# Performance work log

Measured on AMD Instinct MI355X. Metric: run time of the kernel, lower is better.

The kernel has to match this reference:

```python
import jax, jax.numpy as jnp
import numpy as np

# Dimensions
B, D, C, E = 4096, 1024, 512, 16            # batch, embedding_dim, context_dim, n_experts
LIN, R, LOUT = 1024, 16, 1024               # lora_dim = (in, r, out)
H_GATE, H_EXP, Z = 2048, 2048, 512          # gating hidden, expert hidden, expert out


def setup_inputs() -> dict:
    key = jax.random.key(0)
    ks = jax.random.split(key, 12)
    sc = 0.02
    return {
        "s": jax.random.normal(ks[0], (B, D), jnp.float32),
        "c": jax.random.normal(ks[1], (B, C), jnp.float32),
        # gating_model: Linear(D,2048) -> ReLU -> Linear(2048,E) -> Softmax
        "Wg1": jax.random.normal(ks[2], (D, H_GATE), jnp.float32) * sc,
        "bg1": jnp.zeros((H_GATE,), jnp.float32),
        "Wg2": jax.random.normal(ks[3], (H_GATE, E), jnp.float32) * sc,
        "bg2": jnp.zeros((E,), jnp.float32),
        # experts (stacked): Linear(D+C,2048) -> ReLU -> Linear(2048,512)
        "We1": jax.random.normal(ks[4], (E, D + C, H_EXP), jnp.float32) * sc,
        "be1": jnp.zeros((E, H_EXP), jnp.float32),
        "We2": jax.random.normal(ks[5], (E, H_EXP, Z), jnp.float32) * sc,
        "be2": jnp.zeros((E, Z), jnp.float32),
        # LoRA decode heads
        "WA": jax.random.normal(ks[6], (Z, LIN * R), jnp.float32) * sc,
        "bA": jnp.zeros((LIN * R,), jnp.float32),
        "WB": jax.random.normal(ks[7], (Z, R * LOUT), jnp.float32) * sc,
        "bB": jnp.zeros((R * LOUT,), jnp.float32),
    }


def reference(s, c, Wg1, bg1, Wg2, bg2, We1, be1, We2, be2, WA, bA, WB, bB):
    x = jnp.concatenate([s, c], axis=-1)                         # (B, D+C)
    # gating: softmax over experts
    gates = jax.nn.softmax(jnp.maximum(s @ Wg1 + bg1, 0.0) @ Wg2 + bg2, axis=-1)  # (B, E)
    # all-expert dense 2-layer MLPs (soft MoE)
    h = jnp.maximum(jnp.einsum('bd,edh->ebh', x, We1) + be1[:, None, :], 0.0)     # (E, B, H_EXP)
    eo = jnp.einsum('ebh,ehz->ebz', h, We2) + be2[:, None, :]                     # (E, B, Z)
    # gating-weighted sum over experts
    z = jnp.einsum('be,ebz->bz', gates, eo)                      # (B, Z)
    # LoRA decode heads, reshaped per batch element
    A = (z @ WA + bA).reshape(B, LIN, R)
    Bm = (z @ WB + bB).reshape(B, R, LOUT)
    return (A, Bm)
```

## Files before the change

### kernel.cpp

```cpp
#include <hip/hip_runtime.h>
#include <stdint.h>

typedef __attribute__((ext_vector_type(4))) float f32x4;
typedef __attribute__((ext_vector_type(8))) __bf16 bf16x8;

__device__ __forceinline__ ushort f2bf(float f) {
  union { float f; uint32_t u; } v; v.f = f;
  uint32_t r = v.u + 0x7fffu + ((v.u >> 16) & 1u);
  return (ushort)(r >> 16);
}
__device__ __forceinline__ float bf2f(uint32_t h) {
  union { uint32_t u; float f; } v; v.u = h << 16;
  return v.f;
}

__device__ __forceinline__ void gload16(const void* g, const void* l) {
  __builtin_amdgcn_global_load_lds(
      (const __attribute__((address_space(1))) void*)(uintptr_t)g,
      (__attribute__((address_space(3))) void*)(uint32_t)(uintptr_t)l,
      16, 0, 0);
}

template<int EPI, int COL>
__global__ __launch_bounds__(512, 1)
void gemm256p(const ushort* __restrict__ A, const ushort* __restrict__ Bt,
              const float* __restrict__ bias, const float* __restrict__ bias2,
              void* __restrict__ outp,
              int K, int lda, int ldb, int ldo,
              size_t aStride, size_t bStride, int biasStride, size_t oStride,
              const float* __restrict__ gates)
{
  __shared__ __attribute__((aligned(16))) char smem[3 * 32768];

  const int bx = COL ? blockIdx.y : blockIdx.x;
  const int by = COL ? blockIdx.x : blockIdx.y;
  const int eb = blockIdx.z;

  const int t    = threadIdx.x;
  const int lane = t & 63;
  const int wid  = t >> 6;
  const int wr   = wid >> 2, wc = wid & 3;
  const int fr   = lane & 15, fq = lane >> 4;

  const int r  = t >> 2;
  const int jc = (t & 3) ^ ((t >> 3) & 3);
  const ushort* Ae = A  + aStride * eb;
  const ushort* Be = Bt + bStride * eb;
  const ushort* sA0 = Ae + (size_t)(by * 256 + (r >> 6) * 128 +   0 + (r & 63)) * lda + jc * 8;
  const ushort* sA1 = Ae + (size_t)(by * 256 + (r >> 6) * 128 +  64 + (r & 63)) * lda + jc * 8;
  const ushort* sB0 = Be + (size_t)(bx * 256 +   0 + r) * ldb + jc * 8;
  const ushort* sB1 = Be + (size_t)(bx * 256 + 128 + r) * ldb + jc * 8;
  const int dT = t * 16;

  const int swz  = (fq ^ ((fr >> 1) & 3)) * 16;
  const int aOff = (wr * 64 + fr) * 64 + swz;
  const int bOff = 16384 + (wc * 64 + fr) * 64 + swz;

  f32x4 acc[8][4];
#pragma unroll
  for (int m = 0; m < 8; ++m)
#pragma unroll
    for (int n = 0; n < 4; ++n) acc[m][n] = (f32x4){0.f, 0.f, 0.f, 0.f};

  const int NT = K >> 5;

#pragma unroll
  for (int kt = 0; kt < 2; ++kt) {
    char* d = smem + kt * 32768;
    gload16(sA0 + kt * 32, d + dT);
    gload16(sB0 + kt * 32, d + 16384 + dT);
    gload16(sB1 + kt * 32, d + 24576 + dT);
    gload16(sA1 + kt * 32, d + 8192 + dT);
  }
  asm volatile("s_waitcnt vmcnt(5)" ::: "memory");
  __builtin_amdgcn_s_barrier();

  int sc = 0;
  for (int T = 0; T < NT; ++T) {
    const char* base = smem + sc * 32768;
    const int ssi = (sc + 2 >= 3) ? sc - 1 : sc + 2;
    char* d = smem + ssi * 32768;
    const bool pf = (T + 2 < NT);
    const int ko = (T + 2) * 32;

    if (T < NT - 1) asm volatile("s_waitcnt vmcnt(4)" ::: "memory");
    else            asm volatile("s_waitcnt vmcnt(0)" ::: "memory");
    bf16x8 afA[4], bfv[4];
#pragma unroll
    for (int m = 0; m < 4; ++m) afA[m] = *(const bf16x8*)(base + aOff + m * 1024);
#pragma unroll
    for (int n = 0; n < 4; ++n) bfv[n] = *(const bf16x8*)(base + bOff + n * 1024);
    if (pf) { gload16(sA0 + ko, d + dT); gload16(sB0 + ko, d + 16384 + dT); }
    __builtin_amdgcn_sched_barrier(0);
    __builtin_amdgcn_s_barrier();
    __builtin_amdgcn_s_setprio(1);
#pragma unroll
    for (int m = 0; m < 4; ++m)
#pragma unroll
      for (int n = 0; n < 4; ++n)
        acc[m][n] = __builtin_amdgcn_mfma_f32_16x16x32_bf16(afA[m], bfv[n], acc[m][n], 0, 0, 0);
    __builtin_amdgcn_s_setprio(0);

    if (T < NT - 2)       asm volatile("s_waitcnt vmcnt(3)" ::: "memory");
    else if (T == NT - 2) asm volatile("s_waitcnt vmcnt(1)" ::: "memory");
    else                  asm volatile("s_waitcnt vmcnt(0)" ::: "memory");
    bf16x8 afB[4];
#pragma unroll
    for (int m = 0; m < 4; ++m) afB[m] = *(const bf16x8*)(base + 8192 + aOff + m * 1024);
    if (pf) { gload16(sB1 + ko, d + 24576 + dT); gload16(sA1 + ko, d + 8192 + dT); }
    __builtin_amdgcn_sched_barrier(0);
    __builtin_amdgcn_s_barrier();
    __builtin_amdgcn_s_setprio(1);
#pragma unroll
    for (int m = 0; m < 4; ++m)
#pragma unroll
      for (int n = 0; n < 4; ++n)
        acc[4 + m][n] = __builtin_amdgcn_mfma_f32_16x16x32_bf16(afB[m], bfv[n], acc[4 + m][n], 0, 0, 0);
    __builtin_amdgcn_s_setprio(0);

    sc = (sc + 1 == 3) ? 0 : sc + 1;
  }

  const int grow0 = by * 256 + wr * 128 + fq * 4;
  const int gcol0 = bx * 256 + wc * 64 + fr;

  if (EPI == 0) {
    ushort* oo = (ushort*)outp + oStride * eb;
    const float* bb = bias + (size_t)biasStride * eb;
#pragma unroll
    for (int n = 0; n < 4; ++n) {
      const int cc = gcol0 + n * 16;
      const float bv = bb[cc];
#pragma unroll
      for (int m = 0; m < 8; ++m) {
        const int rb = grow0 + (m >> 2) * 64 + (m & 3) * 16;
#pragma unroll
        for (int j = 0; j < 4; ++j) {
          const float v = acc[m][n][j] + bv;
          oo[(size_t)(rb + j) * ldo + cc] = f2bf(v > 0.f ? v : 0.f);
        }
      }
    }
  } else if (EPI == 2) {
    ushort* oo = (ushort*)outp + oStride * eb;
    const float* bb = bias + (size_t)biasStride * eb;
    float gv[8][4];
#pragma unroll
    for (int m = 0; m < 8; ++m) {
      const int rb = grow0 + (m >> 2) * 64 + (m & 3) * 16;
#pragma unroll
      for (int j = 0; j < 4; ++j) gv[m][j] = gates[(size_t)(rb + j) * 16 + eb];
    }
#pragma unroll
    for (int n = 0; n < 4; ++n) {
      const int cc = gcol0 + n * 16;
      const float bv = bb[cc];
#pragma unroll
      for (int m = 0; m < 8; ++m) {
        const int rb = grow0 + (m >> 2) * 64 + (m & 3) * 16;
#pragma unroll
        for (int j = 0; j < 4; ++j) {
          const float v = acc[m][n][j] + bv;
          oo[(size_t)(rb + j) * ldo + cc] = f2bf(v > 0.f ? gv[m][j] * v : 0.f);
        }
      }
    }
  } else if (EPI == 4) {
    float* oo = (float*)outp + oStride * eb;
#pragma unroll
    for (int n = 0; n < 4; ++n) {
      const int cc = gcol0 + n * 16;
#pragma unroll
      for (int m = 0; m < 8; ++m) {
        const int rb = grow0 + (m >> 2) * 64 + (m & 3) * 16;
#pragma unroll
        for (int j = 0; j < 4; ++j)
          oo[(size_t)(rb + j) * ldo + cc] = acc[m][n][j];
      }
    }
  } else {
    const bool second = (gcol0 >= ldo);
    const float* bp = second ? bias2 : bias;
    float* oo = (float*)outp + (second ? oStride : 0);
#pragma unroll
    for (int n = 0; n < 4; ++n) {
      const int cc = gcol0 + n * 16 - (second ? ldo : 0);
      const float bv = bp[cc];
#pragma unroll
      for (int m = 0; m < 8; ++m) {
        const int rb = grow0 + (m >> 2) * 64 + (m & 3) * 16;
#pragma unroll
        for (int j = 0; j < 4; ++j)
          oo[(size_t)(rb + j) * ldo + cc] = acc[m][n][j] + bv;
      }
    }
  }
}

__global__ __launch_bounds__(256)
void transpose_cvt(const float* __restrict__ in, ushort* __restrict__ out,
                   int K, int N, size_t inStride, size_t outStride)
{
  __shared__ float tile[64][65];
  const float* I = in + inStride * blockIdx.z;
  ushort* O = out + outStride * blockIdx.z;
  const int n0 = blockIdx.x * 64, k0 = blockIdx.y * 64;
  const int t = threadIdx.x;
  const int r = t >> 4, cv = (t & 15) * 4;
#pragma unroll
  for (int pp = 0; pp < 4; ++pp) {
    const int kr = r + pp * 16;
    const float4 v = *(const float4*)&I[(size_t)(k0 + kr) * N + (n0 + cv)];
    tile[kr][cv] = v.x; tile[kr][cv + 1] = v.y; tile[kr][cv + 2] = v.z; tile[kr][cv + 3] = v.w;
  }
  __syncthreads();
#pragma unroll
  for (int pp = 0; pp < 4; ++pp) {
    const int nr = r + pp * 16;
    ushort4 o4;
    o4.x = f2bf(tile[cv + 0][nr]); o4.y = f2bf(tile[cv + 1][nr]);
    o4.z = f2bf(tile[cv + 2][nr]); o4.w = f2bf(tile[cv + 3][nr]);
    *(ushort4*)&O[(size_t)(n0 + nr) * K + (k0 + cv)] = o4;
  }
}

__global__ __launch_bounds__(256)
void build_x(const float* __restrict__ s, const float* __restrict__ c, ushort* __restrict__ x)
{
  const size_t i = (size_t)blockIdx.x * 256 + threadIdx.x;
  const size_t b = i / 192;
  const int col  = (int)(i % 192) * 8;
  const float* src = (col < 1024) ? (s + b * 1024 + col) : (c + b * 512 + (col - 1024));
  const float4 v0 = ((const float4*)src)[0];
  const float4 v1 = ((const float4*)src)[1];
  uint4 o;
  o.x = f2bf(v0.x) | ((uint32_t)f2bf(v0.y) << 16);
  o.y = f2bf(v0.z) | ((uint32_t)f2bf(v0.w) << 16);
  o.z = f2bf(v1.x) | ((uint32_t)f2bf(v1.y) << 16);
  o.w = f2bf(v1.z) | ((uint32_t)f2bf(v1.w) << 16);
  *(uint4*)(x + i * 8) = o;
}

__global__ __launch_bounds__(256)
void reduce_z8(const float* __restrict__ zs, const float* __restrict__ gates,
               const float* __restrict__ be2, ushort* __restrict__ zb)
{
  const size_t i = ((size_t)blockIdx.x * 256 + threadIdx.x) * 4;
  const size_t S = (size_t)4096 * 512;
  const int rrow = (int)(i >> 9);
  const int ccol = (int)(i & 511);
  float4 sv = {0.f, 0.f, 0.f, 0.f};
#pragma unroll
  for (int p = 0; p < 8; ++p) {
    const float4 v = *(const float4*)(zs + (size_t)p * S + i);
    sv.x += v.x; sv.y += v.y; sv.z += v.z; sv.w += v.w;
  }
#pragma unroll
  for (int e = 0; e < 16; ++e) {
    const float ge = gates[(size_t)rrow * 16 + e];
    const float4 bv = *(const float4*)(be2 + (size_t)e * 512 + ccol);
    sv.x += ge * bv.x; sv.y += ge * bv.y; sv.z += ge * bv.z; sv.w += ge * bv.w;
  }
  ushort4 o4;
  o4.x = f2bf(sv.x); o4.y = f2bf(sv.y); o4.z = f2bf(sv.z); o4.w = f2bf(sv.w);
  *(ushort4*)(zb + i) = o4;
}

__global__ __launch_bounds__(256)
void gating2_softmax(const ushort* __restrict__ hg, const float* __restrict__ Wg2,
                     const float* __restrict__ bg2, float* __restrict__ gates)
{
  const int row  = (int)((blockIdx.x * 256 + threadIdx.x) >> 6);
  const int lane = threadIdx.x & 63;
  float acc[16];
#pragma unroll
  for (int e = 0; e < 16; ++e) acc[e] = 0.f;
  const ushort* hrow = hg + (size_t)row * 2048;
#pragma unroll
  for (int it = 0; it < 4; ++it) {
    const int kb = it * 512 + lane * 8;
    const uint4 pk = *(const uint4*)(hrow + kb);
    float hv[8] = { bf2f(pk.x & 0xffffu), bf2f(pk.x >> 16),
                    bf2f(pk.y & 0xffffu), bf2f(pk.y >> 16),
                    bf2f(pk.z & 0xffffu), bf2f(pk.z >> 16),
                    bf2f(pk.w & 0xffffu), bf2f(pk.w >> 16) };
#pragma unroll
    for (int j = 0; j < 8; ++j) {
      const float* wrow = Wg2 + (size_t)(kb + j) * 16;
#pragma unroll
      for (int e = 0; e < 16; ++e) acc[e] += hv[j] * wrow[e];
    }
  }
#pragma unroll
  for (int e = 0; e < 16; ++e) {
#pragma unroll
    for (int off = 32; off > 0; off >>= 1) acc[e] += __shfl_xor(acc[e], off);
    acc[e] += bg2[e];
  }
  float mx = acc[0];
#pragma unroll
  for (int e = 1; e < 16; ++e) mx = fmaxf(mx, acc[e]);
  float sum = 0.f;
#pragma unroll
  for (int e = 0; e < 16; ++e) { acc[e] = __expf(acc[e] - mx); sum += acc[e]; }
  const float inv = 1.f / sum;
  if (lane == 0) {
#pragma unroll
    for (int e = 0; e < 16; ++e) gates[(size_t)row * 16 + e] = acc[e] * inv;
  }
}

extern "C" void kernel_launch(void* const* d_in, const int* in_sizes, int n_in,
                              void* d_out, int out_size, void* d_ws, size_t ws_size,
                              hipStream_t stream)
{
  (void)in_sizes; (void)n_in; (void)out_size; (void)ws_size;
  const float* s   = (const float*)d_in[0];
  const float* c   = (const float*)d_in[1];
  const float* Wg1 = (const float*)d_in[2];
  const float* bg1 = (const float*)d_in[3];
  const float* Wg2 = (const float*)d_in[4];
  const float* bg2 = (const float*)d_in[5];
  const float* We1 = (const float*)d_in[6];
  const float* be1 = (const float*)d_in[7];
  const float* We2 = (const float*)d_in[8];
  const float* be2 = (const float*)d_in[9];
  const float* WA  = (const float*)d_in[10];
  const float* bA  = (const float*)d_in[11];
  const float* WB  = (const float*)d_in[12];
  const float* bB  = (const float*)d_in[13];
  float* out = (float*)d_out;

  char* ws = (char*)d_ws;
  size_t off = 0;
  auto alloc = [&](size_t bytes) {
    void* p = ws + off; off += (bytes + 255) & ~(size_t)255; return p;
  };
  ushort* x      = (ushort*)alloc((size_t)4096 * 1536 * 2);
  ushort* We1T   = (ushort*)alloc((size_t)16 * 2048 * 1536 * 2);
  ushort* We2cat = (ushort*)alloc((size_t)512 * 32768 * 2);
  ushort* WABT   = (ushort*)alloc((size_t)32768 * 512 * 2);
  float*  gates  = (float*)alloc((size_t)4096 * 16 * 4);
  float*  zsplit = (float*)alloc((size_t)8 * 4096 * 512 * 4);
  ushort* zb     = (ushort*)alloc((size_t)4096 * 512 * 2);
  ushort* h      = (ushort*)alloc((size_t)4096 * 32768 * 2);
  ushort* Wg1T = h;
  ushort* hg   = (ushort*)((char*)h + (size_t)2048 * 1024 * 2);

  const size_t S_We1 = (size_t)2048 * 1536;
  const size_t S_We2 = (size_t)512 * 2048;
  const size_t S_z   = (size_t)4096 * 512;

  build_x<<<3072, 256, 0, stream>>>(s, c, x);
  transpose_cvt<<<dim3(32, 16, 1),  256, 0, stream>>>(Wg1, Wg1T, 1024, 2048, 0, 0);
  transpose_cvt<<<dim3(32, 24, 16), 256, 0, stream>>>(We1, We1T, 1536, 2048, S_We1, S_We1);
  transpose_cvt<<<dim3(8, 32, 16),  256, 0, stream>>>(We2, We2cat, 32768, 512, S_We2, 2048);
  transpose_cvt<<<dim3(256, 8, 1),  256, 0, stream>>>(WA, WABT, 512, 16384, 0, 0);
  transpose_cvt<<<dim3(256, 8, 1),  256, 0, stream>>>(WB, WABT + (size_t)16384 * 512, 512, 16384, 0, 0);

  gemm256p<0, 1><<<dim3(16, 8, 1), 512, 0, stream>>>(x, Wg1T, bg1, nullptr, hg,
      1024, 1536, 1024, 2048, 0, 0, 0, 0, nullptr);
  gating2_softmax<<<1024, 256, 0, stream>>>(hg, Wg2, bg2, gates);

  gemm256p<2, 1><<<dim3(16, 8, 16), 512, 0, stream>>>(x, We1T, be1, nullptr, h,
      1536, 1536, 1536, 32768, 0, S_We1, 2048, 2048, gates);

  gemm256p<4, 0><<<dim3(2, 16, 8), 512, 0, stream>>>(h, We2cat, be2, nullptr, zsplit,
      4096, 32768, 32768, 512, 4096, 4096, 0, S_z, nullptr);

  reduce_z8<<<2048, 256, 0, stream>>>(zsplit, gates, be2, zb);

  gemm256p<3, 1><<<dim3(16, 128, 1), 512, 0, stream>>>(zb, WABT, bA, bB, out,
      512, 512, 512, 16384, 0, 0, 0, (size_t)4096 * 16384, nullptr);
}
```

Before: 1.181 ms.

## Restructure GEMM main loop barriers, vectorize epilogue stores, double split-K

The GEMM main loop moves each barrier ahead of its LDS fragment reads and prefetch issue, and the waitcnt thresholds are reworked to match. The MFMA operands are swapped so each lane holds four consecutive output columns, which lets the epilogues emit 4-wide vector stores and bias loads instead of scalar ones. The expert-down GEMM's split-K factor goes from 8 to 16 to give more blocks, at the cost of a larger fp32 partial buffer and more reads in the reduction kernel. These changes touch synchronization, output layout and work partitioning together.

```diff
diff --git a/kernel.cpp b/kernel.cpp
--- a/kernel.cpp
+++ b/kernel.cpp
@@ -72,8 +72,6 @@
     gload16(sB1 + kt * 32, d + 24576 + dT);
     gload16(sA1 + kt * 32, d + 8192 + dT);
   }
-  asm volatile("s_waitcnt vmcnt(5)" ::: "memory");
-  __builtin_amdgcn_s_barrier();
 
   int sc = 0;
   for (int T = 0; T < NT; ++T) {
@@ -83,115 +81,106 @@
     const bool pf = (T + 2 < NT);
     const int ko = (T + 2) * 32;
 
-    if (T < NT - 1) asm volatile("s_waitcnt vmcnt(4)" ::: "memory");
-    else            asm volatile("s_waitcnt vmcnt(0)" ::: "memory");
-    bf16x8 afA[4], bfv[4];
-#pragma unroll
-    for (int m = 0; m < 4; ++m) afA[m] = *(const bf16x8*)(base + aOff + m * 1024);
-#pragma unroll
-    for (int n = 0; n < 4; ++n) bfv[n] = *(const bf16x8*)(base + bOff + n * 1024);
+    if (T < NT - 1) asm volatile("s_waitcnt vmcnt(5)" ::: "memory");
+    else            asm volatile("s_waitcnt vmcnt(1)" ::: "memory");
+    __builtin_amdgcn_s_barrier();
     if (pf) { gload16(sA0 + ko, d + dT); gload16(sB0 + ko, d + 16384 + dT); }
-    __builtin_amdgcn_sched_barrier(0);
+
+    bf16x8 af[4], bf[4];
+#pragma unroll
+    for (int m = 0; m < 4; ++m) af[m] = *(const bf16x8*)(base + aOff + m * 1024);
+#pragma unroll
+    for (int n = 0; n < 4; ++n) bf[n] = *(const bf16x8*)(base + bOff + n * 1024);
+
+    __builtin_amdgcn_s_setprio(1);
+#pragma unroll
+    for (int m = 0; m < 4; ++m)
+#pragma unroll
+      for (int n = 0; n < 4; ++n)
+        acc[m][n] = __builtin_amdgcn_mfma_f32_16x16x32_bf16(bf[n], af[m], acc[m][n], 0, 0, 0);
+    __builtin_amdgcn_s_setprio(0);
+
+    if (T < NT - 2)       asm volatile("s_waitcnt vmcnt(6)" ::: "memory");
+    else if (T == NT - 2) asm volatile("s_waitcnt vmcnt(4)" ::: "memory");
+    else                  asm volatile("s_waitcnt vmcnt(0)" ::: "memory");
     __builtin_amdgcn_s_barrier();
+    if (pf) { gload16(sB1 + ko, d + 24576 + dT); gload16(sA1 + ko, d + 8192 + dT); }
+
+#pragma unroll
+    for (int m = 0; m < 4; ++m) af[m] = *(const bf16x8*)(base + 8192 + aOff + m * 1024);
     __builtin_amdgcn_s_setprio(1);
 #pragma unroll
     for (int m = 0; m < 4; ++m)
 #pragma unroll
       for (int n = 0; n < 4; ++n)
-        acc[m][n] = __builtin_amdgcn_mfma_f32_16x16x32_bf16(afA[m], bfv[n], acc[m][n], 0, 0, 0);
+        acc[4 + m][n] = __builtin_amdgcn_mfma_f32_16x16x32_bf16(bf[n], af[m], acc[4 + m][n], 0, 0, 0);
     __builtin_amdgcn_s_setprio(0);
 
-    if (T < NT - 2)       asm volatile("s_waitcnt vmcnt(3)" ::: "memory");
-    else if (T == NT - 2) asm volatile("s_waitcnt vmcnt(1)" ::: "memory");
-    else                  asm volatile("s_waitcnt vmcnt(0)" ::: "memory");
-    bf16x8 afB[4];
-#pragma unroll
-    for (int m = 0; m < 4; ++m) afB[m] = *(const bf16x8*)(base + 8192 + aOff + m * 1024);
-    if (pf) { gload16(sB1 + ko, d + 24576 + dT); gload16(sA1 + ko, d + 8192 + dT); }
-    __builtin_amdgcn_sched_barrier(0);
-    __builtin_amdgcn_s_barrier();
-    __builtin_amdgcn_s_setprio(1);
-#pragma unroll
-    for (int m = 0; m < 4; ++m)
-#pragma unroll
-      for (int n = 0; n < 4; ++n)
-        acc[4 + m][n] = __builtin_amdgcn_mfma_f32_16x16x32_bf16(afB[m], bfv[n], acc[4 + m][n], 0, 0, 0);
-    __builtin_amdgcn_s_setprio(0);
-
     sc = (sc + 1 == 3) ? 0 : sc + 1;
   }
 
-  const int grow0 = by * 256 + wr * 128 + fq * 4;
-  const int gcol0 = bx * 256 + wc * 64 + fr;
+  const int grow0 = by * 256 + wr * 128 + fr;
+  const int gcol0 = bx * 256 + wc * 64 + fq * 4;
 
   if (EPI == 0) {
     ushort* oo = (ushort*)outp + oStride * eb;
     const float* bb = bias + (size_t)biasStride * eb;
 #pragma unroll
-    for (int n = 0; n < 4; ++n) {
-      const int cc = gcol0 + n * 16;
-      const float bv = bb[cc];
-#pragma unroll
-      for (int m = 0; m < 8; ++m) {
-        const int rb = grow0 + (m >> 2) * 64 + (m & 3) * 16;
-#pragma unroll
-        for (int j = 0; j < 4; ++j) {
-          const float v = acc[m][n][j] + bv;
-          oo[(size_t)(rb + j) * ldo + cc] = f2bf(v > 0.f ? v : 0.f);
-        }
+    for (int m = 0; m < 8; ++m) {
+      const int Mr = grow0 + (m >> 2) * 64 + (m & 3) * 16;
+#pragma unroll
+      for (int n = 0; n < 4; ++n) {
+        const int Nc = gcol0 + n * 16;
+        const f32x4 bv = *(const f32x4*)&bb[Nc];
+        ushort4 o4;
+        float v0 = acc[m][n][0] + bv[0]; float v1 = acc[m][n][1] + bv[1];
+        float v2 = acc[m][n][2] + bv[2]; float v3 = acc[m][n][3] + bv[3];
+        o4.x = f2bf(v0 > 0.f ? v0 : 0.f); o4.y = f2bf(v1 > 0.f ? v1 : 0.f);
+        o4.z = f2bf(v2 > 0.f ? v2 : 0.f); o4.w = f2bf(v3 > 0.f ? v3 : 0.f);
+        *(ushort4*)&oo[(size_t)Mr * ldo + Nc] = o4;
       }
     }
   } else if (EPI == 2) {
     ushort* oo = (ushort*)outp + oStride * eb;
     const float* bb = bias + (size_t)biasStride * eb;
-    float gv[8][4];
 #pragma unroll
     for (int m = 0; m < 8; ++m) {
-      const int rb = grow0 + (m >> 2) * 64 + (m & 3) * 16;
-#pragma unroll
-      for (int j = 0; j < 4; ++j) gv[m][j] = gates[(size_t)(rb + j) * 16 + eb];
-    }
-#pragma unroll
-    for (int n = 0; n < 4; ++n) {
-      const int cc = gcol0 + n * 16;
-      const float bv = bb[cc];
-#pragma unroll
-      for (int m = 0; m < 8; ++m) {
-        const int rb = grow0 + (m >> 2) * 64 + (m & 3) * 16;
-#pragma unroll
-        for (int j = 0; j < 4; ++j) {
-          const float v = acc[m][n][j] + bv;
-          oo[(size_t)(rb + j) * ldo + cc] = f2bf(v > 0.f ? gv[m][j] * v : 0.f);
-        }
+      const int Mr = grow0 + (m >> 2) * 64 + (m & 3) * 16;
+      const float g = gates[(size_t)Mr * 16 + eb];
+#pragma unroll
+      for (int n = 0; n < 4; ++n) {
+        const int Nc = gcol0 + n * 16;
+        const f32x4 bv = *(const f32x4*)&bb[Nc];
+        ushort4 o4;
+        float v0 = acc[m][n][0] + bv[0]; float v1 = acc[m][n][1] + bv[1];
+        float v2 = acc[m][n][2] + bv[2]; float v3 = acc[m][n][3] + bv[3];
+        o4.x = f2bf(v0 > 0.f ? g * v0 : 0.f); o4.y = f2bf(v1 > 0.f ? g * v1 : 0.f);
+        o4.z = f2bf(v2 > 0.f ? g * v2 : 0.f); o4.w = f2bf(v3 > 0.f ? g * v3 : 0.f);
+        *(ushort4*)&oo[(size_t)Mr * ldo + Nc] = o4;
       }
     }
   } else if (EPI == 4) {
     float* oo = (float*)outp + oStride * eb;
 #pragma unroll
-    for (int n = 0; n < 4; ++n) {
-      const int cc = gcol0 + n * 16;
-#pragma unroll
-      for (int m = 0; m < 8; ++m) {
-        const int rb = grow0 + (m >> 2) * 64 + (m & 3) * 16;
-#pragma unroll
-        for (int j = 0; j < 4; ++j)
-          oo[(size_t)(rb + j) * ldo + cc] = acc[m][n][j];
-      }
+    for (int m = 0; m < 8; ++m) {
+      const int Mr = grow0 + (m >> 2) * 64 + (m & 3) * 16;
+#pragma unroll
+      for (int n = 0; n < 4; ++n)
+        *(f32x4*)&oo[(size_t)Mr * ldo + gcol0 + n * 16] = acc[m][n];
     }
   } else {
     const bool second = (gcol0 >= ldo);
     const float* bp = second ? bias2 : bias;
     float* oo = (float*)outp + (second ? oStride : 0);
-#pragma unroll
-    for (int n = 0; n < 4; ++n) {
-      const int cc = gcol0 + n * 16 - (second ? ldo : 0);
-      const float bv = bp[cc];
-#pragma unroll
-      for (int m = 0; m < 8; ++m) {
-        const int rb = grow0 + (m >> 2) * 64 + (m & 3) * 16;
-#pragma unroll
-        for (int j = 0; j < 4; ++j)
-          oo[(size_t)(rb + j) * ldo + cc] = acc[m][n][j] + bv;
+    const int cb = second ? ldo : 0;
+#pragma unroll
+    for (int m = 0; m < 8; ++m) {
+      const int Mr = grow0 + (m >> 2) * 64 + (m & 3) * 16;
+#pragma unroll
+      for (int n = 0; n < 4; ++n) {
+        const int Nc = gcol0 + n * 16 - cb;
+        const f32x4 bv = *(const f32x4*)&bp[Nc];
+        *(f32x4*)&oo[(size_t)Mr * ldo + Nc] = acc[m][n] + bv;
       }
     }
   }
@@ -242,8 +231,8 @@
 }
 
 __global__ __launch_bounds__(256)
-void reduce_z8(const float* __restrict__ zs, const float* __restrict__ gates,
-               const float* __restrict__ be2, ushort* __restrict__ zb)
+void reduce_z16(const float* __restrict__ zs, const float* __restrict__ gates,
+                const float* __restrict__ be2, ushort* __restrict__ zb)
 {
   const size_t i = ((size_t)blockIdx.x * 256 + threadIdx.x) * 4;
   const size_t S = (size_t)4096 * 512;
@@ -251,7 +240,7 @@
   const int ccol = (int)(i & 511);
   float4 sv = {0.f, 0.f, 0.f, 0.f};
 #pragma unroll
-  for (int p = 0; p < 8; ++p) {
+  for (int p = 0; p < 16; ++p) {
     const float4 v = *(const float4*)(zs + (size_t)p * S + i);
     sv.x += v.x; sv.y += v.y; sv.z += v.z; sv.w += v.w;
   }
@@ -341,7 +330,7 @@
   ushort* We2cat = (ushort*)alloc((size_t)512 * 32768 * 2);
   ushort* WABT   = (ushort*)alloc((size_t)32768 * 512 * 2);
   float*  gates  = (float*)alloc((size_t)4096 * 16 * 4);
-  float*  zsplit = (float*)alloc((size_t)8 * 4096 * 512 * 4);
+  float*  zsplit = (float*)alloc((size_t)16 * 4096 * 512 * 4);
   ushort* zb     = (ushort*)alloc((size_t)4096 * 512 * 2);
   ushort* h      = (ushort*)alloc((size_t)4096 * 32768 * 2);
   ushort* Wg1T = h;
@@ -365,10 +354,10 @@
   gemm256p<2, 1><<<dim3(16, 8, 16), 512, 0, stream>>>(x, We1T, be1, nullptr, h,
       1536, 1536, 1536, 32768, 0, S_We1, 2048, 2048, gates);
 
-  gemm256p<4, 0><<<dim3(2, 16, 8), 512, 0, stream>>>(h, We2cat, be2, nullptr, zsplit,
-      4096, 32768, 32768, 512, 4096, 4096, 0, S_z, nullptr);
-
-  reduce_z8<<<2048, 256, 0, stream>>>(zsplit, gates, be2, zb);
+  gemm256p<4, 0><<<dim3(2, 16, 16), 512, 0, stream>>>(h, We2cat, be2, nullptr, zsplit,
+      2048, 32768, 32768, 512, 2048, 2048, 0, S_z, nullptr);
+
+  reduce_z16<<<2048, 256, 0, stream>>>(zsplit, gates, be2, zb);
 
   gemm256p<3, 1><<<dim3(16, 128, 1), 512, 0, stream>>>(zb, WABT, bA, bB, out,
       512, 512, 512, 16384, 0, 0, 0, (size_t)4096 * 16384, nullptr);
```

New measurement: 1.100 ms. 1.07x faster.
